# Kernel optimization log

Hardware: AMD Instinct MI355X
Metric: run time of the kernel (lower is better)

## Reference

```python
import jax, jax.numpy as jnp
import numpy as np
import math

DIM = 2048
N_BRANCH = 4
B, L = 2, 4096
NC = N_BRANCH * DIM
N2 = N_BRANCH * N_BRANCH
EPS = 1e-20
NUM_ITER = 20


def sinkhorn_knopp(matrix):
    # matrix: [B, L, n, n] -> doubly-stochastic via 20 alternating row/col normalizations
    K = jnp.exp(matrix)
    def body(i, K):
        K = K / (K.sum(axis=-1, keepdims=True) + EPS)
        K = K / (K.sum(axis=-2, keepdims=True) + EPS)
        return K
    return jax.lax.fori_loop(0, NUM_ITER, body, K)


def setup_inputs() -> dict:
    key = jax.random.key(0)
    k1, k2 = jax.random.split(key)
    hidden_states = jax.random.normal(k1, (B, L, N_BRANCH, DIM), dtype=jnp.float32)
    # phi: nn.Linear(nc, n2 + 2n, bias=False); torch weight layout [out, in]
    W_phi = jax.random.normal(k2, (N2 + 2 * N_BRANCH, NC), dtype=jnp.float32) * 0.02
    a = jnp.ones((3,), dtype=jnp.float32) * 0.01
    b = jnp.zeros((N2 + 2 * N_BRANCH,), dtype=jnp.float32)
    return {"hidden_states": hidden_states, "W_phi": W_phi, "a": a, "b": b}


def reference(hidden_states, W_phi, a, b):
    Bsz, Lsz, n, d = hidden_states.shape
    nc = n * d
    hs_flat = hidden_states.reshape(Bsz, Lsz, nc)                     # [B, L, nc]
    r = jnp.linalg.norm(hs_flat, axis=-1, keepdims=True) / math.sqrt(nc)  # [B, L, 1]
    H = jnp.einsum('blc,oc->blo', hs_flat, W_phi)                     # [B, L, n2+2n]
    inv_r = 1.0 / r
    H_pre = jax.nn.sigmoid(inv_r * H[..., :n] * a[0] + b[:n])                 # [B, L, n]
    H_post = 2.0 * jax.nn.sigmoid(inv_r * H[..., n:2 * n] * a[1] + b[n:2 * n])  # [B, L, n]
    H_res = inv_r * H[..., 2 * n:] * a[2] + b[2 * n:]                 # [B, L, n*n]
    H_res = sinkhorn_knopp(H_res.reshape(Bsz, Lsz, n, n))             # [B, L, n, n]
    # width connection
    h_pre = jnp.einsum('bln,blnd->bld', H_pre, hidden_states)         # [B, L, d]
    h_res = jnp.einsum('blmn,blnd->blmd', H_res, hidden_states)       # [B, L, n, d]
    # depth connection (processed single-branch signal stands in for attention/FFN output;
    # here the identity of h_pre is used so the full graph is exercised)
    h_post = H_post[..., None] * h_pre[:, :, None, :]                 # [B, L, n, d]
    output = h_post + h_res
    return output
```

## Files before the change

### kernel.cpp

```cpp
#include <hip/hip_runtime.h>
#include <math.h>


__global__ __launch_bounds__(256)
void mhc_fused(const float* __restrict__ hs,
               const float* __restrict__ Wphi,
               const float* __restrict__ av,
               const float* __restrict__ bv,
               float* __restrict__ out)
{
    const int tid  = threadIdx.x;
    const int wave = tid >> 6;
    const int lane = tid & 63;
    const long long t0 = (long long)blockIdx.x * 8;

    __shared__ float Hlds[8][25];
    __shared__ float preL[8][4];
    __shared__ float postL[8][4];
    __shared__ float resL[8][16];

    const int obase = wave * 6;
    const float4* hs4 = reinterpret_cast<const float4*>(hs + t0 * 8192);
    const float4* W4  = reinterpret_cast<const float4*>(Wphi) + (size_t)obase * 2048;

    float acc[8][6];
    float accN[8];
#pragma unroll
    for (int t = 0; t < 8; ++t) {
        accN[t] = 0.f;
#pragma unroll
        for (int o = 0; o < 6; ++o) acc[t][o] = 0.f;
    }

    for (int i = 0; i < 32; ++i) {
        const int k4 = lane + (i << 6);
        float4 h[8];
#pragma unroll
        for (int t = 0; t < 8; ++t) h[t] = hs4[t * 2048 + k4];
#pragma unroll
        for (int o = 0; o < 6; ++o) {
            const float4 w = W4[o * 2048 + k4];
#pragma unroll
            for (int t = 0; t < 8; ++t)
                acc[t][o] += w.x * h[t].x + w.y * h[t].y + w.z * h[t].z + w.w * h[t].w;
        }
        if (wave == 0) {
#pragma unroll
            for (int t = 0; t < 8; ++t)
                accN[t] += h[t].x * h[t].x + h[t].y * h[t].y
                         + h[t].z * h[t].z + h[t].w * h[t].w;
        }
    }

#pragma unroll
    for (int t = 0; t < 8; ++t) {
#pragma unroll
        for (int o = 0; o < 6; ++o) {
            float v = acc[t][o];
            v += __shfl_xor(v, 32); v += __shfl_xor(v, 16); v += __shfl_xor(v, 8);
            v += __shfl_xor(v, 4);  v += __shfl_xor(v, 2);  v += __shfl_xor(v, 1);
            if (lane == 0) Hlds[t][obase + o] = v;
        }
    }
    if (wave == 0) {
#pragma unroll
        for (int t = 0; t < 8; ++t) {
            float v = accN[t];
            v += __shfl_xor(v, 32); v += __shfl_xor(v, 16); v += __shfl_xor(v, 8);
            v += __shfl_xor(v, 4);  v += __shfl_xor(v, 2);  v += __shfl_xor(v, 1);
            if (lane == 0) Hlds[t][24] = v;
        }
    }
    __syncthreads();

    if (tid < 128) {
        const int t = tid >> 4;
        const int e = tid & 15;
        const float normsq = Hlds[t][24];
        const float inv_r  = sqrtf(8192.0f / normsq);
        const float a0 = av[0], a1 = av[1], a2 = av[2];

        float K = expf(inv_r * Hlds[t][8 + e] * a2 + bv[8 + e]);
        for (int it = 0; it < 20; ++it) {
            float rs = K + __shfl_xor(K, 1);
            rs += __shfl_xor(rs, 2);
            K = K / (rs + 1e-20f);
            float cs = K + __shfl_xor(K, 4);
            cs += __shfl_xor(cs, 8);
            K = K / (cs + 1e-20f);
        }
        resL[t][e] = K;

        if (e < 4) {
            float xp = inv_r * Hlds[t][e] * a0 + bv[e];
            preL[t][e] = 1.0f / (1.0f + expf(-xp));
            float xq = inv_r * Hlds[t][4 + e] * a1 + bv[4 + e];
            postL[t][e] = 2.0f / (1.0f + expf(-xq));
        }
    }
    __syncthreads();

    const float4* hsr  = reinterpret_cast<const float4*>(hs + t0 * 8192);
    float4*       out4 = reinterpret_cast<float4*>(out) + t0 * 2048;

    for (int t = 0; t < 8; ++t) {
        float pre[4], post[4], res[16];
#pragma unroll
        for (int n = 0; n < 4; ++n) { pre[n] = preL[t][n]; post[n] = postL[t][n]; }
#pragma unroll
        for (int e = 0; e < 16; ++e) res[e] = resL[t][e];

#pragma unroll
        for (int ii = 0; ii < 2; ++ii) {
            const int c4 = tid + (ii << 8);
            float4 h[4];
#pragma unroll
            for (int n = 0; n < 4; ++n) h[n] = hsr[t * 2048 + n * 512 + c4];

            float4 hp;
            hp.x = pre[0]*h[0].x + pre[1]*h[1].x + pre[2]*h[2].x + pre[3]*h[3].x;
            hp.y = pre[0]*h[0].y + pre[1]*h[1].y + pre[2]*h[2].y + pre[3]*h[3].y;
            hp.z = pre[0]*h[0].z + pre[1]*h[1].z + pre[2]*h[2].z + pre[3]*h[3].z;
            hp.w = pre[0]*h[0].w + pre[1]*h[1].w + pre[2]*h[2].w + pre[3]*h[3].w;

#pragma unroll
            for (int m = 0; m < 4; ++m) {
                const float r0 = res[m*4+0], r1 = res[m*4+1], r2 = res[m*4+2], r3 = res[m*4+3];
                const float pm = post[m];
                float4 o;
                o.x = pm*hp.x + r0*h[0].x + r1*h[1].x + r2*h[2].x + r3*h[3].x;
                o.y = pm*hp.y + r0*h[0].y + r1*h[1].y + r2*h[2].y + r3*h[3].y;
                o.z = pm*hp.z + r0*h[0].z + r1*h[1].z + r2*h[2].z + r3*h[3].z;
                o.w = pm*hp.w + r0*h[0].w + r1*h[1].w + r2*h[2].w + r3*h[3].w;
                out4[t * 2048 + m * 512 + c4] = o;
            }
        }
    }
}

extern "C" void kernel_launch(void* const* d_in, const int* in_sizes, int n_in,
                              void* d_out, int out_size, void* d_ws, size_t ws_size,
                              hipStream_t stream) {
    const float* hs  = (const float*)d_in[0];
    const float* Wp  = (const float*)d_in[1];
    const float* av  = (const float*)d_in[2];
    const float* bv  = (const float*)d_in[3];
    float* out = (float*)d_out;

    const int tokens = in_sizes[0] / 8192;
    const int blocks = tokens / 8;

    mhc_fused<<<blocks, 256, 0, stream>>>(hs, Wp, av, bv, out);
}
```

Before: 510.7 us.

## Split fused kernel into gate and recombine kernels with double-buffered loads

Splits the single fused kernel in two. The first kernel computes the projection, norm and Sinkhorn gates and writes them to a workspace buffer. The second kernel, launched with one block per token, re-reads hidden_states and applies the gates, which gives many more blocks for the bandwidth-bound recombine phase. The projection loop also now double-buffers its hidden-state loads to overlap memory with FMA work. This costs an extra kernel launch, a second read of hidden_states that may be served from the large last-level cache, and higher register pressure in the gate kernel.

```diff
diff --git a/kernel.cpp b/kernel.cpp
--- a/kernel.cpp
+++ b/kernel.cpp
@@ -3,11 +3,11 @@
 
 
 __global__ __launch_bounds__(256)
-void mhc_fused(const float* __restrict__ hs,
+void mhc_gates(const float* __restrict__ hs,
                const float* __restrict__ Wphi,
                const float* __restrict__ av,
                const float* __restrict__ bv,
-               float* __restrict__ out)
+               float* __restrict__ gates)
 {
     const int tid  = threadIdx.x;
     const int wave = tid >> 6;
@@ -15,9 +15,6 @@
     const long long t0 = (long long)blockIdx.x * 8;
 
     __shared__ float Hlds[8][25];
-    __shared__ float preL[8][4];
-    __shared__ float postL[8][4];
-    __shared__ float resL[8][16];
 
     const int obase = wave * 6;
     const float4* hs4 = reinterpret_cast<const float4*>(hs + t0 * 8192);
@@ -32,24 +29,40 @@
         for (int o = 0; o < 6; ++o) acc[t][o] = 0.f;
     }
 
-    for (int i = 0; i < 32; ++i) {
-        const int k4 = lane + (i << 6);
-        float4 h[8];
+    float4 hA[8], hB[8];
 #pragma unroll
-        for (int t = 0; t < 8; ++t) h[t] = hs4[t * 2048 + k4];
+    for (int t = 0; t < 8; ++t) hA[t] = hs4[t * 2048 + lane];
+
+    auto fma_blk = [&](const float4* hb, int k4) {
 #pragma unroll
         for (int o = 0; o < 6; ++o) {
             const float4 w = W4[o * 2048 + k4];
 #pragma unroll
             for (int t = 0; t < 8; ++t)
-                acc[t][o] += w.x * h[t].x + w.y * h[t].y + w.z * h[t].z + w.w * h[t].w;
+                acc[t][o] += w.x * hb[t].x + w.y * hb[t].y
+                           + w.z * hb[t].z + w.w * hb[t].w;
         }
         if (wave == 0) {
 #pragma unroll
             for (int t = 0; t < 8; ++t)
-                accN[t] += h[t].x * h[t].x + h[t].y * h[t].y
-                         + h[t].z * h[t].z + h[t].w * h[t].w;
+                accN[t] += hb[t].x * hb[t].x + hb[t].y * hb[t].y
+                         + hb[t].z * hb[t].z + hb[t].w * hb[t].w;
         }
+    };
+
+    for (int i = 0; i < 32; i += 2) {
+        {
+            const int kn = lane + ((i + 1) << 6);
+#pragma unroll
+            for (int t = 0; t < 8; ++t) hB[t] = hs4[t * 2048 + kn];
+        }
+        fma_blk(hA, lane + (i << 6));
+        if (i + 2 < 32) {
+            const int kn = lane + ((i + 2) << 6);
+#pragma unroll
+            for (int t = 0; t < 8; ++t) hA[t] = hs4[t * 2048 + kn];
+        }
+        fma_blk(hB, lane + ((i + 1) << 6));
     }
 
 #pragma unroll
@@ -79,6 +92,7 @@
         const float normsq = Hlds[t][24];
         const float inv_r  = sqrtf(8192.0f / normsq);
         const float a0 = av[0], a1 = av[1], a2 = av[2];
+        float* g = gates + (t0 + t) * 24;
 
         float K = expf(inv_r * Hlds[t][8 + e] * a2 + bv[8 + e]);
         for (int it = 0; it < 20; ++it) {
@@ -89,51 +103,59 @@
             cs += __shfl_xor(cs, 8);
             K = K / (cs + 1e-20f);
         }
-        resL[t][e] = K;
+        g[8 + e] = K;
 
         if (e < 4) {
             float xp = inv_r * Hlds[t][e] * a0 + bv[e];
-            preL[t][e] = 1.0f / (1.0f + expf(-xp));
+            g[e] = 1.0f / (1.0f + expf(-xp));
             float xq = inv_r * Hlds[t][4 + e] * a1 + bv[4 + e];
-            postL[t][e] = 2.0f / (1.0f + expf(-xq));
+            g[4 + e] = 2.0f / (1.0f + expf(-xq));
         }
     }
+}
+
+__global__ __launch_bounds__(256)
+void mhc_recombine(const float* __restrict__ hs,
+                   const float* __restrict__ gates,
+                   float* __restrict__ out)
+{
+    const long long tok = blockIdx.x;
+    __shared__ float g[24];
+    if (threadIdx.x < 24) g[threadIdx.x] = gates[tok * 24 + threadIdx.x];
     __syncthreads();
 
-    const float4* hsr  = reinterpret_cast<const float4*>(hs + t0 * 8192);
-    float4*       out4 = reinterpret_cast<float4*>(out) + t0 * 2048;
+    float pre[4], post[4], res[16];
+#pragma unroll
+    for (int n = 0; n < 4; ++n) { pre[n] = g[n]; post[n] = g[4 + n]; }
+#pragma unroll
+    for (int e = 0; e < 16; ++e) res[e] = g[8 + e];
 
-    for (int t = 0; t < 8; ++t) {
-        float pre[4], post[4], res[16];
-#pragma unroll
-        for (int n = 0; n < 4; ++n) { pre[n] = preL[t][n]; post[n] = postL[t][n]; }
-#pragma unroll
-        for (int e = 0; e < 16; ++e) res[e] = resL[t][e];
+    const float4* h4 = reinterpret_cast<const float4*>(hs) + tok * 2048;
+    float4*       o4 = reinterpret_cast<float4*>(out) + tok * 2048;
 
 #pragma unroll
-        for (int ii = 0; ii < 2; ++ii) {
-            const int c4 = tid + (ii << 8);
-            float4 h[4];
+    for (int ii = 0; ii < 2; ++ii) {
+        const int c4 = threadIdx.x + (ii << 8);
+        float4 h[4];
 #pragma unroll
-            for (int n = 0; n < 4; ++n) h[n] = hsr[t * 2048 + n * 512 + c4];
+        for (int n = 0; n < 4; ++n) h[n] = h4[n * 512 + c4];
 
-            float4 hp;
-            hp.x = pre[0]*h[0].x + pre[1]*h[1].x + pre[2]*h[2].x + pre[3]*h[3].x;
-            hp.y = pre[0]*h[0].y + pre[1]*h[1].y + pre[2]*h[2].y + pre[3]*h[3].y;
-            hp.z = pre[0]*h[0].z + pre[1]*h[1].z + pre[2]*h[2].z + pre[3]*h[3].z;
-            hp.w = pre[0]*h[0].w + pre[1]*h[1].w + pre[2]*h[2].w + pre[3]*h[3].w;
+        float4 hp;
+        hp.x = pre[0]*h[0].x + pre[1]*h[1].x + pre[2]*h[2].x + pre[3]*h[3].x;
+        hp.y = pre[0]*h[0].y + pre[1]*h[1].y + pre[2]*h[2].y + pre[3]*h[3].y;
+        hp.z = pre[0]*h[0].z + pre[1]*h[1].z + pre[2]*h[2].z + pre[3]*h[3].z;
+        hp.w = pre[0]*h[0].w + pre[1]*h[1].w + pre[2]*h[2].w + pre[3]*h[3].w;
 
 #pragma unroll
-            for (int m = 0; m < 4; ++m) {
-                const float r0 = res[m*4+0], r1 = res[m*4+1], r2 = res[m*4+2], r3 = res[m*4+3];
-                const float pm = post[m];
-                float4 o;
-                o.x = pm*hp.x + r0*h[0].x + r1*h[1].x + r2*h[2].x + r3*h[3].x;
-                o.y = pm*hp.y + r0*h[0].y + r1*h[1].y + r2*h[2].y + r3*h[3].y;
-                o.z = pm*hp.z + r0*h[0].z + r1*h[1].z + r2*h[2].z + r3*h[3].z;
-                o.w = pm*hp.w + r0*h[0].w + r1*h[1].w + r2*h[2].w + r3*h[3].w;
-                out4[t * 2048 + m * 512 + c4] = o;
-            }
+        for (int m = 0; m < 4; ++m) {
+            const float r0 = res[m*4+0], r1 = res[m*4+1], r2 = res[m*4+2], r3 = res[m*4+3];
+            const float pm = post[m];
+            float4 o;
+            o.x = pm*hp.x + r0*h[0].x + r1*h[1].x + r2*h[2].x + r3*h[3].x;
+            o.y = pm*hp.y + r0*h[0].y + r1*h[1].y + r2*h[2].y + r3*h[3].y;
+            o.z = pm*hp.z + r0*h[0].z + r1*h[1].z + r2*h[2].z + r3*h[3].z;
+            o.w = pm*hp.w + r0*h[0].w + r1*h[1].w + r2*h[2].w + r3*h[3].w;
+            o4[m * 512 + c4] = o;
         }
     }
 }
@@ -145,10 +167,11 @@
     const float* Wp  = (const float*)d_in[1];
     const float* av  = (const float*)d_in[2];
     const float* bv  = (const float*)d_in[3];
-    float* out = (float*)d_out;
+    float* out   = (float*)d_out;
+    float* gates = (float*)d_ws;
 
     const int tokens = in_sizes[0] / 8192;
-    const int blocks = tokens / 8;
 
-    mhc_fused<<<blocks, 256, 0, stream>>>(hs, Wp, av, bv, out);
+    mhc_gates<<<tokens / 8, 256, 0, stream>>>(hs, Wp, av, bv, gates);
+    mhc_recombine<<<tokens, 256, 0, stream>>>(hs, gates, out);
 }
```

Result: slower. 528.8 us (+3.6%).
